# Kernel tuning notes

Measured on AMD Instinct MI355X. Metric: run time of the kernel, lower is better.

Reference implementation:

```python
import jax, jax.numpy as jnp
import numpy as np

NUM_GT = 25      # num_gt_lesions (init kwarg); labels 1..25 all present in gt
NUM_PRED = 40    # number of predicted CC labels (labels 0..40 in pred)
SMOOTH = 1.0
VOL = (256, 256, 256)


def setup_inputs() -> dict:
    key = jax.random.key(0)
    k1, k2 = jax.random.split(key)
    # pred holds integer-valued connected-component labels stored as float
    # (the original applies sigmoid to it and compares values for identity).
    pred = jax.random.randint(k1, VOL, 0, NUM_PRED + 1).astype(jnp.float32)
    gt = jax.random.randint(k2, VOL, 0, NUM_GT + 1).astype(jnp.int32)
    return {"pred": pred, "gt": gt}


def _instance_dice(pred, gt):
    # Original: s = sigmoid(pred); all unique/isin/!=0 tests are on s.
    # sigmoid is injective => value equality on s == label equality on pred;
    # sigmoid(x) != 0 always  => every `!= 0` filter in the original is a no-op
    # (in particular pred label 0 participates, since sigmoid(0)=0.5).
    lbl = jax.lax.stop_gradient(jnp.round(pred)).astype(jnp.int32)  # pred CC ids
    g = gt.astype(jnp.int32)

    # Joint histogram counts[p, c] = #voxels with pred==p and gt==c.
    combined = (lbl * (NUM_GT + 1) + g).ravel()
    counts = jnp.zeros((NUM_PRED + 1) * (NUM_GT + 1), jnp.float32)
    counts = counts.at[combined].add(1.0).reshape(NUM_PRED + 1, NUM_GT + 1)

    gt_sizes = counts[:, 1:].sum(axis=0)            # [L] |gt == c| for c=1..L
    present = gt_sizes > 0
    num_gt = present.sum()                          # torch.unique(gt[gt!=0]).size(0)

    overlap = counts[:, 1:] > 0                     # [P+1, L] pred label p hits comp c
    pred_sizes = counts.sum(axis=1)                 # [P+1] |pred == p|
    union_size = (overlap * pred_sizes[:, None]).sum(axis=0)  # |pred_tmp| per comp
    # pred_tmp covers every voxel of the gt component => intersection = gt_sizes
    dice = 2.0 * gt_sizes / (union_size + gt_sizes + SMOOTH)
    lesion_dice = jnp.where(present, dice, 0.0).sum()

    tp_any = (overlap & present[None, :]).any(axis=1)  # pred labels collected in tp
    fp = ((pred_sizes > 0) & ~tp_any).sum()            # pred labels missing all gt comps
    return lesion_dice / (num_gt + fp)


def reference(pred, gt):
    return _instance_dice(pred, gt)
```

## Files before the change

### kernel.cpp

```cpp
#include <hip/hip_runtime.h>
#include <hip/hip_bf16.h>

#define NUM_GT 25
#define NUM_PRED 40
#define PAD 32

#define GT_W(b)  ((b) * PAD)
#define PR_W(p)  ((25 + (p)) * PAD)
#define OV_W(p)  ((65 + (p)) * PAD)
#define WS_WORDS (106 * PAD)

#define GRID  1024
#define BLOCK 256
#define TILE  2048

#if defined(__has_builtin)
#  if __has_builtin(__builtin_amdgcn_sad_u8)
#    define SAD(A, W, K) (A) = __builtin_amdgcn_sad_u8((W), (K), (A))
#  endif
#endif
#ifndef SAD
#  define SAD(A, W, K) asm("v_sad_u8 %0, %1, %2, %0" : "+v"(A) : "v"(W), "s"(K))
#endif

#define AS1 __attribute__((address_space(1)))
#define AS3 __attribute__((address_space(3)))

__device__ __forceinline__ void stage_tile(
    const unsigned* __restrict__ gsrc, unsigned* ldst, int wid, int lane)
{
#if defined(__has_builtin) && __has_builtin(__builtin_amdgcn_global_load_lds)
    const unsigned* s0 = gsrc + wid * 512 + lane * 4;
    unsigned* d0 = ldst + wid * 512;
    __builtin_amdgcn_global_load_lds((const AS1 unsigned*)s0,
                                     (AS3 unsigned*)d0, 16, 0, 0);
    __builtin_amdgcn_global_load_lds((const AS1 unsigned*)(s0 + 256),
                                     (AS3 unsigned*)(d0 + 256), 16, 0, 0);
#else
    *(uint4*)(ldst + wid * 512 + lane * 4) =
        *(const uint4*)(gsrc + wid * 512 + lane * 4);
    *(uint4*)(ldst + wid * 512 + 256 + lane * 4) =
        *(const uint4*)(gsrc + wid * 512 + 256 + lane * 4);
#endif
}

__global__ __launch_bounds__(BLOCK) void hist_kernel(
    const float* __restrict__ pred, const int* __restrict__ gt,
    unsigned* __restrict__ ws, int n)
{
    __shared__ unsigned lgt[2][TILE];
    __shared__ unsigned lpr[2][TILE];
    __shared__ unsigned sovl[64];
    __shared__ unsigned shist[66];

    const int tid  = threadIdx.x;
    const int lane = tid & 63;
    const int wid  = tid >> 6;

    if (tid < 64) sovl[tid] = 0u;
    if (tid < 66) shist[tid] = 0u;

    unsigned acc[66];
    #pragma unroll
    for (int j = 0; j < 66; ++j) acc[j] = 0u;

    const unsigned* __restrict__ gu = (const unsigned*)gt;
    const unsigned* __restrict__ pu = (const unsigned*)pred;
    const int ntiles = n / TILE;

    int t = blockIdx.x;
    int cur = 0;
    if (t < ntiles) {
        stage_tile(gu + (size_t)t * TILE, &lgt[0][0], wid, lane);
        stage_tile(pu + (size_t)t * TILE, &lpr[0][0], wid, lane);
    }
    __syncthreads();

    for (; t < ntiles; t += GRID) {
        const int tn = t + GRID;
        if (tn < ntiles) {
            stage_tile(gu + (size_t)tn * TILE, &lgt[cur ^ 1][0], wid, lane);
            stage_tile(pu + (size_t)tn * TILE, &lpr[cur ^ 1][0], wid, lane);
        }

        const uint4* g4 = (const uint4*)(&lgt[cur][0] + wid * 512);
        const uint4* p4 = (const uint4*)(&lpr[cur][0] + wid * 512);
        #pragma unroll
        for (int h = 0; h < 2; ++h) {
            uint4 gw = g4[h * 64 + lane];
            uint4 pw = p4[h * 64 + lane];
            unsigned b0 = (unsigned)__uint_as_float(pw.x);
            unsigned b1 = (unsigned)__uint_as_float(pw.y);
            unsigned b2 = (unsigned)__uint_as_float(pw.z);
            unsigned b3 = (unsigned)__uint_as_float(pw.w);

            atomicOr(&sovl[b0 & 63], 1u << (gw.x & 31));
            atomicOr(&sovl[b1 & 63], 1u << (gw.y & 31));
            atomicOr(&sovl[b2 & 63], 1u << (gw.z & 31));
            atomicOr(&sovl[b3 & 63], 1u << (gw.w & 31));

            unsigned G = gw.x | (gw.y << 8) | (gw.z << 16) | (gw.w << 24);
            unsigned P = b0 | (b1 << 8) | (b2 << 16) | (b3 << 24);
            #pragma unroll
            for (int b = 0; b < 25; ++b) {
                const unsigned K = (unsigned)(b * 0x01010101u);
                SAD(acc[b], G, K);
            }
            #pragma unroll
            for (int b = 0; b < 40; ++b) {
                const unsigned K = (unsigned)(b * 0x01010101u);
                SAD(acc[25 + b], P, K);
            }
        }

        __syncthreads();
        cur ^= 1;
    }

    if (blockIdx.x == 0 && tid == 0) {
        for (int v = ntiles * TILE; v < n; ++v) {
            int p = (int)pred[v];
            int g = gt[v];
            for (int b = 0; b < 25; ++b) atomicAdd(&ws[GT_W(b)], (unsigned)abs(g - b));
            for (int b = 0; b < 40; ++b) atomicAdd(&ws[PR_W(b)], (unsigned)abs(p - b));
            atomicOr(&ws[OV_W(min(max(p, 0), NUM_PRED))], 1u << (g & 31));
        }
    }

    unsigned (*stash)[16][34] = (unsigned(*)[16][34])(&lgt[0][0]);
    #pragma unroll
    for (int jp = 0; jp < 33; ++jp) {
        unsigned v = acc[2 * jp] | (acc[2 * jp + 1] << 16);
        v += __shfl_down(v, 32, 64);
        v += __shfl_down(v, 16, 64);
        if (lane < 16) stash[wid][lane][jp] = v;
    }
    __syncthreads();

    for (int i = tid; i < 33 * 16; i += BLOCK) {
        int jp = i >> 4, sl = i & 15;
        unsigned a = stash[0][sl][jp] + stash[1][sl][jp]
                   + stash[2][sl][jp] + stash[3][sl][jp];
        unsigned lo = a & 0xFFFFu, hi = a >> 16;
        lo += __shfl_down(lo, 8, 16);  hi += __shfl_down(hi, 8, 16);
        lo += __shfl_down(lo, 4, 16);  hi += __shfl_down(hi, 4, 16);
        lo += __shfl_down(lo, 2, 16);  hi += __shfl_down(hi, 2, 16);
        lo += __shfl_down(lo, 1, 16);  hi += __shfl_down(hi, 1, 16);
        if (sl == 0) {
            if (lo) atomicAdd(&shist[2 * jp], lo);
            if (hi && 2 * jp + 1 < 65) atomicAdd(&shist[2 * jp + 1], hi);
        }
    }
    __syncthreads();

    for (int i = tid; i < 65; i += BLOCK) {
        unsigned s = shist[i];
        if (s) atomicAdd(&ws[i * PAD], s);
    }
    if (tid < 41) {
        unsigned v = sovl[tid];
        if (v) atomicOr(&ws[OV_W(tid)], v);
    }
}

__global__ __launch_bounds__(64) void finish_kernel(
    const unsigned* __restrict__ ws, float* __restrict__ out, int n)
{
    __shared__ long long gg[25], gp[40], psz[41];
    __shared__ unsigned ov[41];
    const int lane = threadIdx.x;
    if (lane < 25) gg[lane] = (long long)ws[GT_W(lane)];
    if (lane < 40) gp[lane] = (long long)ws[PR_W(lane)];
    if (lane < 41) ov[lane] = ws[OV_W(lane)];
    __syncthreads();

    const long long N = n, Sg = gg[0], Sp = gp[0];

    if (lane < 41) {
        int P = lane;
        long long f;
        if (P == 0)       f = (N - gp[0] + gp[1]) / 2;
        else if (P <= 38) f = (gp[P - 1] - 2 * gp[P] + gp[P + 1]) / 2;
        else if (P == 39) f = (gp[38] - 2 * gp[39] + (40 * N - Sp)) / 2;
        else              f = (gp[39] - 39 * N + Sp) / 2;
        psz[P] = f;
    }
    __syncthreads();

    double dice = 0.0;
    int present = 0;
    if (lane < 25) {
        int L = lane + 1;
        long long gs;
        if (L <= 23)      gs = (gg[L - 1] - 2 * gg[L] + gg[L + 1]) / 2;
        else if (L == 24) gs = (gg[23] - 2 * gg[24] + (25 * N - Sg)) / 2;
        else              gs = (gg[24] - 24 * N + Sg) / 2;
        if (gs > 0) {
            present = 1;
            double un = 0.0;
            const unsigned bit = 1u << L;
            for (int p = 0; p < 41; ++p)
                if (ov[p] & bit) un += (double)psz[p];
            dice = 2.0 * (double)gs / (un + (double)gs + 1.0);
        }
    }
    int fp = 0;
    if (lane < 41) {
        if (psz[lane] > 0 && (ov[lane] & 0x3FFFFFEu) == 0) fp = 1;
    }

    int num_gt = __popcll(__ballot(present != 0));
    int nfp    = __popcll(__ballot(fp != 0));
    #pragma unroll
    for (int o = 32; o >= 1; o >>= 1) dice += __shfl_xor(dice, o, 64);

    if (lane == 0) out[0] = (float)(dice / (double)(num_gt + nfp));
}

extern "C" void kernel_launch(void* const* d_in, const int* in_sizes, int n_in,
                              void* d_out, int out_size, void* d_ws, size_t ws_size,
                              hipStream_t stream) {
    const float* pred = (const float*)d_in[0];
    const int* gt = (const int*)d_in[1];
    float* out = (float*)d_out;
    unsigned* ws = (unsigned*)d_ws;
    const int n = in_sizes[0];

    hipMemsetAsync(ws, 0, WS_WORDS * sizeof(unsigned), stream);

    hist_kernel<<<GRID, BLOCK, 0, stream>>>(pred, gt, ws, n);
    finish_kernel<<<1, 64, 0, stream>>>(ws, out, n);
}
```

Baseline: 45.40 us.

## Replace block barriers with per-wave vmcnt waits and two-tile-ahead prefetch

The histogram loop no longer calls __syncthreads per tile. Each wave now stages and reads only its own 512-word LDS slice and uses explicit s_waitcnt vmcnt/lgkmcnt counts to know when its async global-to-LDS loads have landed. The next stage is issued two tiles ahead into the buffer just consumed. This removes block-wide synchronisation and lets waves drift independently to hide memory latency. The cost is reliance on hand-counted waitcnt values, which would break if the compiler emits other vector memory ops in the loop or if the non-builtin fallback path is used.

Result: no change. 45.39 us (-0.0%).

```diff
diff --git a/kernel.cpp b/kernel.cpp
--- a/kernel.cpp
+++ b/kernel.cpp
@@ -26,23 +26,14 @@
 #define AS1 __attribute__((address_space(1)))
 #define AS3 __attribute__((address_space(3)))
 
-__device__ __forceinline__ void stage_tile(
-    const unsigned* __restrict__ gsrc, unsigned* ldst, int wid, int lane)
-{
 #if defined(__has_builtin) && __has_builtin(__builtin_amdgcn_global_load_lds)
-    const unsigned* s0 = gsrc + wid * 512 + lane * 4;
-    unsigned* d0 = ldst + wid * 512;
-    __builtin_amdgcn_global_load_lds((const AS1 unsigned*)s0,
-                                     (AS3 unsigned*)d0, 16, 0, 0);
-    __builtin_amdgcn_global_load_lds((const AS1 unsigned*)(s0 + 256),
-                                     (AS3 unsigned*)(d0 + 256), 16, 0, 0);
+#define GLOAD(SRC, DST) \
+    __builtin_amdgcn_global_load_lds((const AS1 unsigned*)(SRC), \
+                                     (AS3 unsigned*)(DST), 16, 0, 0)
 #else
-    *(uint4*)(ldst + wid * 512 + lane * 4) =
-        *(const uint4*)(gsrc + wid * 512 + lane * 4);
-    *(uint4*)(ldst + wid * 512 + 256 + lane * 4) =
-        *(const uint4*)(gsrc + wid * 512 + 256 + lane * 4);
+#define GLOAD(SRC, DST)  \
+    (*(uint4*)((DST) + (threadIdx.x & 63) * 4) = *(const uint4*)(SRC))
 #endif
-}
 
 __global__ __launch_bounds__(BLOCK) void hist_kernel(
     const float* __restrict__ pred, const int* __restrict__ gt,
@@ -67,24 +58,33 @@
     const unsigned* __restrict__ gu = (const unsigned*)gt;
     const unsigned* __restrict__ pu = (const unsigned*)pred;
     const int ntiles = n / TILE;
-
-    int t = blockIdx.x;
-    int cur = 0;
-    if (t < ntiles) {
-        stage_tile(gu + (size_t)t * TILE, &lgt[0][0], wid, lane);
-        stage_tile(pu + (size_t)t * TILE, &lpr[0][0], wid, lane);
-    }
-    __syncthreads();
-
-    for (; t < ntiles; t += GRID) {
-        const int tn = t + GRID;
-        if (tn < ntiles) {
-            stage_tile(gu + (size_t)tn * TILE, &lgt[cur ^ 1][0], wid, lane);
-            stage_tile(pu + (size_t)tn * TILE, &lpr[cur ^ 1][0], wid, lane);
-        }
-
-        const uint4* g4 = (const uint4*)(&lgt[cur][0] + wid * 512);
-        const uint4* p4 = (const uint4*)(&lpr[cur][0] + wid * 512);
+    const int nt = (ntiles > (int)blockIdx.x)
+                 ? (ntiles - (int)blockIdx.x + GRID - 1) / GRID : 0;
+
+    __syncthreads();
+
+    #define STAGE(K)                                                          \
+    do {                                                                      \
+        const size_t base = ((size_t)blockIdx.x + (size_t)(K) * GRID) * TILE  \
+                          + wid * 512;                                        \
+        const unsigned* sg = gu + base + lane * 4;                            \
+        unsigned* dg = &lgt[(K) & 1][0] + wid * 512;                          \
+        GLOAD(sg, dg); GLOAD(sg + 256, dg + 256);                             \
+        const unsigned* sp = pu + base + lane * 4;                            \
+        unsigned* dp = &lpr[(K) & 1][0] + wid * 512;                          \
+        GLOAD(sp, dp); GLOAD(sp + 256, dp + 256);                             \
+    } while (0)
+
+    if (nt > 0) STAGE(0);
+    if (nt > 1) STAGE(1);
+
+    for (int k = 0; k < nt; ++k) {
+        if (k + 1 < nt) asm volatile("s_waitcnt vmcnt(4)" ::: "memory");
+        else            asm volatile("s_waitcnt vmcnt(0)" ::: "memory");
+        __builtin_amdgcn_sched_barrier(0);
+
+        const uint4* g4 = (const uint4*)(&lgt[k & 1][0] + wid * 512);
+        const uint4* p4 = (const uint4*)(&lpr[k & 1][0] + wid * 512);
         #pragma unroll
         for (int h = 0; h < 2; ++h) {
             uint4 gw = g4[h * 64 + lane];
@@ -113,9 +113,13 @@
             }
         }
 
-        __syncthreads();
-        cur ^= 1;
-    }
+        if (k + 2 < nt) {
+            asm volatile("s_waitcnt lgkmcnt(0)" ::: "memory");
+            __builtin_amdgcn_sched_barrier(0);
+            STAGE(k + 2);
+        }
+    }
+    #undef STAGE
 
     if (blockIdx.x == 0 && tid == 0) {
         for (int v = ntiles * TILE; v < n; ++v) {
@@ -127,6 +131,7 @@
         }
     }
 
+    __syncthreads();
     unsigned (*stash)[16][34] = (unsigned(*)[16][34])(&lgt[0][0]);
     #pragma unroll
     for (int jp = 0; jp < 33; ++jp) {
```
